# Performance work log

Hardware: AMD Instinct MI355X
Metric: run time of the kernel (lower is better)

## Reference

```python
import jax, jax.numpy as jnp
import numpy as np

WIN = (7, 7)
N_TOK = WIN[0] * WIN[1]          # 49
DIM = 512
HEADS = 16
B_WIN = 2048                     # num_windows * batch
NW = 64                          # windows per image (mask leading dim)


def _relative_position_index():
    # Mirrors the torch __init__ coords computation.
    coords = np.stack(np.meshgrid(np.arange(WIN[0]), np.arange(WIN[1]), indexing='ij'))  # [2,Wh,Ww]
    flat = coords.reshape(2, -1)                                   # [2, N]
    rel = flat[:, :, None] - flat[:, None, :]                      # [2, N, N]
    rel = rel.transpose(1, 2, 0).astype(np.int32)                  # [N, N, 2]
    rel[:, :, 0] += WIN[0] - 1
    rel[:, :, 1] += WIN[1] - 1
    rel[:, :, 0] *= 2 * WIN[1] - 1
    return jnp.asarray(rel.sum(-1), dtype=jnp.int32)               # [N, N]


def setup_inputs() -> dict:
    key = jax.random.key(0)
    ks = jax.random.split(key, 7)
    x = jax.random.normal(ks[0], (B_WIN, N_TOK, DIM), jnp.float32)
    w_qkv = jax.random.normal(ks[1], (3 * DIM, DIM), jnp.float32) * 0.02
    b_qkv = jax.random.normal(ks[2], (3 * DIM,), jnp.float32) * 0.02
    w_proj = jax.random.normal(ks[3], (DIM, DIM), jnp.float32) * 0.02
    b_proj = jax.random.normal(ks[4], (DIM,), jnp.float32) * 0.02
    bias_table = jax.random.normal(ks[5], ((2 * WIN[0] - 1) * (2 * WIN[1] - 1), HEADS), jnp.float32) * 0.02
    rel_index = _relative_position_index()
    # shift-window mask: 0 for allowed, -100 for masked (Swin convention)
    mask = jnp.where(jax.random.bernoulli(ks[6], 0.1, (NW, N_TOK, N_TOK)), -100.0, 0.0).astype(jnp.float32)
    return {"x": x, "w_qkv": w_qkv, "b_qkv": b_qkv, "w_proj": w_proj,
            "b_proj": b_proj, "bias_table": bias_table, "rel_index": rel_index, "mask": mask}


def reference(x, w_qkv, b_qkv, w_proj, b_proj, bias_table, rel_index, mask):
    B_, N, C = x.shape
    H = HEADS
    hd = C // H
    scale = hd ** -0.5
    # qkv projection: [B, N, 3, H, hd] -> q,k,v each [B, H, N, hd]
    qkv = (jnp.einsum('bnc,oc->bno', x, w_qkv) + b_qkv)
    qkv = qkv.reshape(B_, N, 3, H, hd).transpose(2, 0, 3, 1, 4)
    q, k, v = qkv[0], qkv[1], qkv[2]
    attn = jnp.einsum('bhnd,bhmd->bhnm', q * scale, k)             # [B, H, N, N]
    # relative position bias gather: [N*N] -> [N, N, H] -> [H, N, N]
    rpb = bias_table[rel_index.reshape(-1)].reshape(N, N, H).transpose(2, 0, 1)
    attn = attn + rpb[None]
    nW = mask.shape[0]
    attn = attn.reshape(B_ // nW, nW, H, N, N) + mask[None, :, None]
    attn = attn.reshape(B_, H, N, N)
    attn = jax.nn.softmax(attn, axis=-1)
    out = jnp.einsum('bhnm,bhmd->bhnd', attn, v)                   # [B, H, N, hd]
    out = out.transpose(0, 2, 1, 3).reshape(B_, N, C)
    out = jnp.einsum('bnc,oc->bno', out, w_proj) + b_proj
    return out
```

## Files before the change

kernel.cpp:

```cpp
#include <hip/hip_runtime.h>
#include <stdint.h>

typedef unsigned short u16;
typedef unsigned int u32;
typedef unsigned long long u64;
typedef __attribute__((ext_vector_type(4))) u16 u16x4;
typedef __attribute__((ext_vector_type(8))) u16 u16x8;
typedef __attribute__((ext_vector_type(2))) u32 u32x2;
typedef __attribute__((ext_vector_type(8))) short bf16x8;
typedef __attribute__((ext_vector_type(4))) float f32x4;

#define DEVFN __device__ __forceinline__

DEVFN u16 f2bf(float f) {
  union { float f; u32 u; } x; x.f = f;
  u32 u = x.u;
  return (u16)((u + 0x7fffu + ((u >> 16) & 1u)) >> 16);
}
DEVFN float bf2f(u16 v) {
  union { u32 u; float f; } x; x.u = ((u32)v) << 16;
  return x.f;
}

__global__ void cvt_kernel(const float* __restrict__ in, u16* __restrict__ out, int n4) {
  const int stride = gridDim.x * blockDim.x;
  for (int i = blockIdx.x * blockDim.x + threadIdx.x; i < n4; i += stride) {
    float4 v = reinterpret_cast<const float4*>(in)[i];
    u16x4 o;
    o.x = f2bf(v.x); o.y = f2bf(v.y); o.z = f2bf(v.z); o.w = f2bf(v.w);
    reinterpret_cast<u16x4*>(out)[i] = o;
  }
}

__global__ void pbb_kernel(const float* __restrict__ bt, const int* __restrict__ ri,
                           u16* __restrict__ pbb) {
  const int h = blockIdx.x;
  for (int t = threadIdx.x; t < 4096; t += 256) {
    const int i = t >> 6, j = t & 63;
    float v = 0.f;
    if (i < 49 && j < 49) v = bt[ri[i * 49 + j] * 16 + h];
    pbb[h * 4096 + t] = f2bf(v);
  }
}

__global__ void mbits_kernel(const float* __restrict__ mask, u64* __restrict__ mb) {
  const int w = blockIdx.x;
  const int i = threadIdx.x;
  u64 m = ~0ull << 49;
  if (i < 49) {
    for (int j = 0; j < 49; ++j)
      if (mask[w * 2401 + i * 49 + j] < -1.0f) m |= 1ull << j;
  } else {
    m = ~0ull;
  }
  mb[w * 64 + i] = m;
}

#define WAIT_LGKM0 asm volatile("s_waitcnt lgkmcnt(0)" ::: "memory")
#define WAIT_VM8   asm volatile("s_waitcnt vmcnt(8)" ::: "memory")
#define WAIT_VM0   asm volatile("s_waitcnt vmcnt(0)" ::: "memory")
#define SCHEDB     __builtin_amdgcn_sched_barrier(0)
#define BARRIER    __builtin_amdgcn_s_barrier()
#define MFMA(a, b, c) __builtin_amdgcn_mfma_f32_16x16x32_bf16(a, b, c, 0, 0, 0)

template <int MODE, int NTILES, int MCHUNK>
__global__ __launch_bounds__(512) void gemm_kernel(
    const u16* __restrict__ A, const u16* __restrict__ Bt,
    const float* __restrict__ bias, void* __restrict__ Out, int ldo) {
  extern __shared__ u16 smem[];
  const int tid = threadIdx.x;
  const int lane = tid & 63;
  const int wid = tid >> 6;
  const int bid = blockIdx.x;
  const int xcd = bid & 7;
  const int slot = bid >> 3;
  const int m0 = (xcd * MCHUNK + slot / NTILES) * 256;
  const int n0 = (slot % NTILES) * 256;
  const int wr = wid >> 2, wc = wid & 3;
  const int l15 = lane & 15, lg = lane >> 4;
  const int rg0 = tid >> 3;
  const int sl0 = tid & 7;

  f32x4 acc[8][4] = {};

  u16* const sA0 = smem;
  u16* const sB0 = smem + 16384;
  u16* const sA1 = smem + 32768;
  u16* const sB1 = smem + 49152;

#define STAGE(kt_, sa_, sb_)                                                   \
  {                                                                            \
    _Pragma("unroll") for (int i = 0; i < 4; ++i) {                            \
      const int rg = i * 64 + rg0;                                             \
      const int kc = sl0 ^ (rg & 7);                                           \
      const u16* ga = A + (size_t)(m0 + rg) * 512 + (kt_) * 64 + kc * 8;       \
      __builtin_amdgcn_global_load_lds(                                        \
          (const __attribute__((address_space(1))) void*)ga,                   \
          (__attribute__((address_space(3))) void*)((sa_) + i * 4096 + wid * 512), \
          16, 0, 0);                                                           \
    }                                                                          \
    _Pragma("unroll") for (int i = 0; i < 4; ++i) {                            \
      const int rg = i * 64 + rg0;                                             \
      const int kc = sl0 ^ (rg & 7);                                           \
      const u16* gb = Bt + (size_t)(n0 + rg) * 512 + (kt_) * 64 + kc * 8;      \
      __builtin_amdgcn_global_load_lds(                                        \
          (const __attribute__((address_space(1))) void*)gb,                   \
          (__attribute__((address_space(3))) void*)((sb_) + i * 4096 + wid * 512), \
          16, 0, 0);                                                           \
    }                                                                          \
  }

#define RDA(dst, sa_, mi, ks)                                                  \
  {                                                                            \
    const int row_ = wr * 128 + (mi) * 16 + l15;                               \
    dst = *reinterpret_cast<const bf16x8*>(                                    \
        (sa_) + row_ * 64 + ((((ks) * 4 + lg) ^ (row_ & 7)) << 3));            \
  }
#define RDB(dst, sb_, ni, ks)                                                  \
  {                                                                            \
    const int row_ = wc * 64 + (ni) * 16 + l15;                                \
    dst = *reinterpret_cast<const bf16x8*>(                                    \
        (sb_) + row_ * 64 + ((((ks) * 4 + lg) ^ (row_ & 7)) << 3));            \
  }

  STAGE(0, sA0, sB0);
  STAGE(1, sA1, sB1);
  WAIT_VM8; SCHEDB;
  BARRIER; SCHEDB;

#pragma unroll
  for (int kt = 0; kt < 8; ++kt) {
    u16* const sa = (kt & 1) ? sA1 : sA0;
    u16* const sb = (kt & 1) ? sB1 : sB0;
    bf16x8 a0[4][2], a1[4][2], b0[2][2], b1[2][2];

#pragma unroll
    for (int mi = 0; mi < 4; ++mi) { RDA(a0[mi][0], sa, mi, 0); RDA(a0[mi][1], sa, mi, 1); }
#pragma unroll
    for (int ni = 0; ni < 2; ++ni) { RDB(b0[ni][0], sb, ni, 0); RDB(b0[ni][1], sb, ni, 1); }
    WAIT_LGKM0; SCHEDB;
    __builtin_amdgcn_s_setprio(1);
#pragma unroll
    for (int mi = 0; mi < 4; ++mi)
#pragma unroll
      for (int ni = 0; ni < 2; ++ni)
#pragma unroll
        for (int ks = 0; ks < 2; ++ks)
          acc[mi][ni] = MFMA(a0[mi][ks], b0[ni][ks], acc[mi][ni]);
    __builtin_amdgcn_s_setprio(0); SCHEDB;

#pragma unroll
    for (int ni = 0; ni < 2; ++ni) { RDB(b1[ni][0], sb, ni + 2, 0); RDB(b1[ni][1], sb, ni + 2, 1); }
    WAIT_LGKM0; SCHEDB;
    __builtin_amdgcn_s_setprio(1);
#pragma unroll
    for (int mi = 0; mi < 4; ++mi)
#pragma unroll
      for (int ni = 0; ni < 2; ++ni)
#pragma unroll
        for (int ks = 0; ks < 2; ++ks)
          acc[mi][ni + 2] = MFMA(a0[mi][ks], b1[ni][ks], acc[mi][ni + 2]);
    __builtin_amdgcn_s_setprio(0); SCHEDB;

#pragma unroll
    for (int mi = 0; mi < 4; ++mi) { RDA(a1[mi][0], sa, mi + 4, 0); RDA(a1[mi][1], sa, mi + 4, 1); }
    WAIT_LGKM0; SCHEDB;
    __builtin_amdgcn_s_setprio(1);
#pragma unroll
    for (int mi = 0; mi < 4; ++mi)
#pragma unroll
      for (int ni = 0; ni < 2; ++ni)
#pragma unroll
        for (int ks = 0; ks < 2; ++ks)
          acc[mi + 4][ni + 2] = MFMA(a1[mi][ks], b1[ni][ks], acc[mi + 4][ni + 2]);
    __builtin_amdgcn_s_setprio(0); SCHEDB;

    BARRIER; SCHEDB;
    if (kt < 6) STAGE(kt + 2, sa, sb);

    __builtin_amdgcn_s_setprio(1);
#pragma unroll
    for (int mi = 0; mi < 4; ++mi)
#pragma unroll
      for (int ni = 0; ni < 2; ++ni)
#pragma unroll
        for (int ks = 0; ks < 2; ++ks)
          acc[mi + 4][ni] = MFMA(a1[mi][ks], b0[ni][ks], acc[mi + 4][ni]);
    __builtin_amdgcn_s_setprio(0); SCHEDB;

    if (kt < 6) { WAIT_VM8; }
    else if (kt == 6) { WAIT_VM0; }
    SCHEDB;
    if (kt < 7) { BARRIER; SCHEDB; }
  }
#undef STAGE
#undef RDA
#undef RDB

#pragma unroll
  for (int mi = 0; mi < 8; ++mi) {
#pragma unroll
    for (int ni = 0; ni < 4; ++ni) {
      const int col = n0 + wc * 64 + ni * 16 + l15;
      const float bv = bias[col];
      const int rbase = m0 + wr * 128 + mi * 16 + lg * 4;
#pragma unroll
      for (int r = 0; r < 4; ++r) {
        const float v = acc[mi][ni][r] + bv;
        if (MODE == 0) {
          ((u16*)Out)[(size_t)(rbase + r) * ldo + col] = f2bf(v);
        } else {
          ((float*)Out)[(size_t)(rbase + r) * ldo + col] = v;
        }
      }
    }
  }
}

__global__ __launch_bounds__(256) void attn_kernel(
    const u16* __restrict__ qkv, const u16* __restrict__ pbb,
    const u64* __restrict__ mbits, u16* __restrict__ attn_out) {
  const int w = threadIdx.x >> 6;
  const int lane = threadIdx.x & 63;
  const int b = blockIdx.x >> 2;
  const int h = ((blockIdx.x & 3) << 2) | w;
  const int l15 = lane & 15, lg = lane >> 4;
  const int lg4 = lg * 4;

  __shared__ u16 sVT[4][32][72];
  u16 (*vt)[72] = sVT[w];

  for (int i = lane; i < 1152; i += 64) ((u32*)vt)[i] = 0;

  const size_t rowbase = (size_t)b * (49 * 1536) + h * 32;

  for (int c = lane; c < 196; c += 64) {
    const int n = c >> 2, dg = c & 3;
    u16x8 vv = *reinterpret_cast<const u16x8*>(qkv + rowbase + (size_t)n * 1536 + 1024 + dg * 8);
    const int pin = ((n >> 5) << 5) | ((((n >> 2) & 3)) << 3) | (((n >> 4) & 1) << 2) | (n & 3);
#pragma unroll
    for (int j = 0; j < 8; ++j) vt[dg * 8 + j][pin] = vv[j];
  }

  bf16x8 aq[4], bk[4];
#pragma unroll
  for (int t = 0; t < 4; ++t) {
    const int i = t * 16 + l15;
    const int r = i < 49 ? i : 48;
    const size_t ro = rowbase + (size_t)r * 1536 + lg * 8;
    aq[t] = *reinterpret_cast<const bf16x8*>(qkv + ro);
    bk[t] = *reinterpret_cast<const bf16x8*>(qkv + ro + 512);
  }

  const u64* mwb = mbits + ((b & 63) << 6);
  u64 mb[4];
#pragma unroll
  for (int qt = 0; qt < 4; ++qt) mb[qt] = mwb[qt * 16 + l15];

  bf16x8 bv[2][2];
#pragma unroll
  for (int ni = 0; ni < 2; ++ni)
#pragma unroll
    for (int ks = 0; ks < 2; ++ks)
      bv[ni][ks] = *reinterpret_cast<const bf16x8*>(&vt[ni * 16 + l15][ks * 32 + lg * 8]);

  const float scale = 0.17677669529663687f;
  const u16* pbh = pbb + (h << 12);
  const size_t obase = (size_t)b * 49 * 512 + h * 32;

#pragma unroll
  for (int qt = 0; qt < 4; ++qt) {
    f32x4 sT[4] = {};
#pragma unroll
    for (int kt = 0; kt < 4; ++kt)
      sT[kt] = __builtin_amdgcn_mfma_f32_16x16x32_bf16(bk[kt], aq[qt], sT[kt], 0, 0, 0);

    const int i = qt * 16 + l15;
    const u16* pr = pbh + i * 64 + lg4;
    float v[4][4];
    float mx = -3e38f;
#pragma unroll
    for (int kt = 0; kt < 4; ++kt) {
      u16x4 pv = *reinterpret_cast<const u16x4*>(pr + kt * 16);
      const u32 nib = (u32)(mb[qt] >> (kt * 16 + lg4)) & 0xFu;
#pragma unroll
      for (int r = 0; r < 4; ++r) {
        float val = fmaf(sT[kt][r], scale, bf2f(pv[r]));
        if (nib & (1u << r)) val -= 100.f;
        if (kt == 3 && (lg4 + r) >= 1) val = -1e30f;
        v[kt][r] = val;
        mx = fmaxf(mx, val);
      }
    }
    mx = fmaxf(mx, __shfl_xor(mx, 16));
    mx = fmaxf(mx, __shfl_xor(mx, 32));
    float sum = 0.f;
#pragma unroll
    for (int kt = 0; kt < 4; ++kt)
#pragma unroll
      for (int r = 0; r < 4; ++r) {
        const float e = __expf(v[kt][r] - mx);
        v[kt][r] = e;
        sum += e;
      }
    sum += __shfl_xor(sum, 16);
    sum += __shfl_xor(sum, 32);
    const float rinv = 1.0f / sum;

    bf16x8 ap[2];
#pragma unroll
    for (int ks = 0; ks < 2; ++ks) {
      u32 w0 = (u32)f2bf(v[2 * ks][0] * rinv) | ((u32)f2bf(v[2 * ks][1] * rinv) << 16);
      u32 w1 = (u32)f2bf(v[2 * ks][2] * rinv) | ((u32)f2bf(v[2 * ks][3] * rinv) << 16);
      u32 w2 = (u32)f2bf(v[2 * ks + 1][0] * rinv) | ((u32)f2bf(v[2 * ks + 1][1] * rinv) << 16);
      u32 w3 = (u32)f2bf(v[2 * ks + 1][2] * rinv) | ((u32)f2bf(v[2 * ks + 1][3] * rinv) << 16);
      union { u32 u[4]; bf16x8 b; } pk;
      pk.u[0] = w0; pk.u[1] = w1; pk.u[2] = w2; pk.u[3] = w3;
      ap[ks] = pk.b;
    }

    f32x4 o[2] = {};
#pragma unroll
    for (int ks = 0; ks < 2; ++ks)
#pragma unroll
      for (int ni = 0; ni < 2; ++ni)
        o[ni] = __builtin_amdgcn_mfma_f32_16x16x32_bf16(ap[ks], bv[ni][ks], o[ni], 0, 0, 0);

#pragma unroll
    for (int r = 0; r < 4; ++r) {
      const int iq = qt * 16 + lg4 + r;
      if (iq < 49) {
#pragma unroll
        for (int ni = 0; ni < 2; ++ni)
          attn_out[obase + (size_t)iq * 512 + ni * 16 + l15] = f2bf(o[ni][r]);
      }
    }
  }
}

extern "C" void kernel_launch(void* const* d_in, const int* in_sizes, int n_in,
                              void* d_out, int out_size, void* d_ws, size_t ws_size,
                              hipStream_t stream) {
  (void)in_sizes; (void)n_in; (void)out_size; (void)ws_size;
  const float* x          = (const float*)d_in[0];
  const float* w_qkv      = (const float*)d_in[1];
  const float* b_qkv      = (const float*)d_in[2];
  const float* w_proj     = (const float*)d_in[3];
  const float* b_proj     = (const float*)d_in[4];
  const float* bias_table = (const float*)d_in[5];
  const int*   rel_index  = (const int*)d_in[6];
  const float* mask       = (const float*)d_in[7];

  u16* ws     = (u16*)d_ws;
  u16* xbf    = ws;
  u16* qkv    = ws + 51380224;
  u16* wqkvb  = qkv + 154140672;
  u16* wprojb = wqkvb + 786432;
  u16* pbb    = wprojb + 262144;
  u64* mbits  = (u64*)(pbb + 65536);

  (void)hipFuncSetAttribute((const void*)gemm_kernel<0, 6, 49>,
                            hipFuncAttributeMaxDynamicSharedMemorySize, 131072);
  (void)hipFuncSetAttribute((const void*)gemm_kernel<1, 2, 49>,
                            hipFuncAttributeMaxDynamicSharedMemorySize, 131072);

  cvt_kernel<<<2048, 256, 0, stream>>>(x, xbf, 51380224 / 4);
  cvt_kernel<<<192, 256, 0, stream>>>(w_qkv, wqkvb, 786432 / 4);
  cvt_kernel<<<64, 256, 0, stream>>>(w_proj, wprojb, 262144 / 4);
  pbb_kernel<<<16, 256, 0, stream>>>(bias_table, rel_index, pbb);
  mbits_kernel<<<64, 64, 0, stream>>>(mask, mbits);

  gemm_kernel<0, 6, 49><<<2352, 512, 131072, stream>>>(xbf, wqkvb, b_qkv, qkv, 1536);
  attn_kernel<<<8192, 256, 0, stream>>>(qkv, pbb, mbits, xbf);
  gemm_kernel<1, 2, 49><<<784, 512, 131072, stream>>>(xbf, wprojb, b_proj, d_out, 512);
}
```

Measured before the change: 514.2 us.

## Interleave global-to-LDS prefetch in quarter-tile chunks across MFMA phases

Splits each K-tile's global_load_lds staging into four half-panel chunks, issued one per MFMA phase and offset by three phases. The goal is to spread memory traffic evenly across the compute loop rather than issuing all loads at once after a barrier. This adds several extra workgroup barriers per K-step and changes the vmcnt waits. The offset scheduling must avoid overwriting a buffer that is still being read, which is a correctness risk.

```diff
diff --git a/kernel.cpp b/kernel.cpp
--- a/kernel.cpp
+++ b/kernel.cpp
@@ -57,7 +57,8 @@
 }
 
 #define WAIT_LGKM0 asm volatile("s_waitcnt lgkmcnt(0)" ::: "memory")
-#define WAIT_VM8   asm volatile("s_waitcnt vmcnt(8)" ::: "memory")
+#define WAIT_LGKM8 asm volatile("s_waitcnt lgkmcnt(8)" ::: "memory")
+#define WAIT_VM2   asm volatile("s_waitcnt vmcnt(2)" ::: "memory")
 #define WAIT_VM0   asm volatile("s_waitcnt vmcnt(0)" ::: "memory")
 #define SCHEDB     __builtin_amdgcn_sched_barrier(0)
 #define BARRIER    __builtin_amdgcn_s_barrier()
@@ -83,61 +84,62 @@
 
   f32x4 acc[8][4] = {};
 
-  u16* const sA0 = smem;
-  u16* const sB0 = smem + 16384;
-  u16* const sA1 = smem + 32768;
-  u16* const sB1 = smem + 49152;
-
-#define STAGE(kt_, sa_, sb_)                                                   \
+#define STAGE_RAW(kt_, hp_)                                                    \
   {                                                                            \
-    _Pragma("unroll") for (int i = 0; i < 4; ++i) {                            \
-      const int rg = i * 64 + rg0;                                             \
-      const int kc = sl0 ^ (rg & 7);                                           \
-      const u16* ga = A + (size_t)(m0 + rg) * 512 + (kt_) * 64 + kc * 8;       \
+    const u16* srcp_ = ((hp_) < 2)                                             \
+        ? (A + (size_t)(m0 + ((hp_) & 1) * 128) * 512)                         \
+        : (Bt + (size_t)(n0 + ((hp_) & 1) * 128) * 512);                       \
+    u16* dst_ = smem + ((kt_) & 1) * 32768 + (hp_) * 8192;                     \
+    _Pragma("unroll") for (int i_ = 0; i_ < 2; ++i_) {                         \
+      const int rg_ = i_ * 64 + rg0;                                           \
+      const int kc_ = sl0 ^ (rg_ & 7);                                         \
+      const u16* g_ = srcp_ + (size_t)rg_ * 512 + (kt_) * 64 + kc_ * 8;        \
       __builtin_amdgcn_global_load_lds(                                        \
-          (const __attribute__((address_space(1))) void*)ga,                   \
-          (__attribute__((address_space(3))) void*)((sa_) + i * 4096 + wid * 512), \
+          (const __attribute__((address_space(1))) void*)g_,                   \
+          (__attribute__((address_space(3))) void*)(dst_ + i_ * 4096 + wid * 512), \
           16, 0, 0);                                                           \
     }                                                                          \
-    _Pragma("unroll") for (int i = 0; i < 4; ++i) {                            \
-      const int rg = i * 64 + rg0;                                             \
-      const int kc = sl0 ^ (rg & 7);                                           \
-      const u16* gb = Bt + (size_t)(n0 + rg) * 512 + (kt_) * 64 + kc * 8;      \
-      __builtin_amdgcn_global_load_lds(                                        \
-          (const __attribute__((address_space(1))) void*)gb,                   \
-          (__attribute__((address_space(3))) void*)((sb_) + i * 4096 + wid * 512), \
-          16, 0, 0);                                                           \
-    }                                                                          \
-  }
-
-#define RDA(dst, sa_, mi, ks)                                                  \
+  }
+
+#define STG(g_)                                                                \
+  if ((g_) >= 3 && (g_) < 27) {                                                \
+    const int s_ = (g_) - 3;                                                   \
+    STAGE_RAW(2 + s_ / 4, s_ & 3);                                             \
+  }
+
+#define RDA(dst, mi_, ks_)                                                     \
   {                                                                            \
-    const int row_ = wr * 128 + (mi) * 16 + l15;                               \
+    const int row_ = wr * 128 + (mi_) * 16 + l15;                              \
     dst = *reinterpret_cast<const bf16x8*>(                                    \
-        (sa_) + row_ * 64 + ((((ks) * 4 + lg) ^ (row_ & 7)) << 3));            \
-  }
-#define RDB(dst, sb_, ni, ks)                                                  \
+        smem + cb + row_ * 64 + ((((ks_) * 4 + lg) ^ (row_ & 7)) << 3));       \
+  }
+#define RDB(dst, ni_, ks_)                                                     \
   {                                                                            \
-    const int row_ = wc * 64 + (ni) * 16 + l15;                                \
+    const int row_ = wc * 64 + (ni_) * 16 + l15;                               \
     dst = *reinterpret_cast<const bf16x8*>(                                    \
-        (sb_) + row_ * 64 + ((((ks) * 4 + lg) ^ (row_ & 7)) << 3));            \
-  }
-
-  STAGE(0, sA0, sB0);
-  STAGE(1, sA1, sB1);
-  WAIT_VM8; SCHEDB;
+        smem + cb + 16384 + row_ * 64 + ((((ks_) * 4 + lg) ^ (row_ & 7)) << 3)); \
+  }
+
+#pragma unroll
+  for (int hp = 0; hp < 4; ++hp) STAGE_RAW(0, hp);
+#pragma unroll
+  for (int hp = 0; hp < 4; ++hp) STAGE_RAW(1, hp);
+  WAIT_VM0; SCHEDB;
   BARRIER; SCHEDB;
 
 #pragma unroll
   for (int kt = 0; kt < 8; ++kt) {
-    u16* const sa = (kt & 1) ? sA1 : sA0;
-    u16* const sb = (kt & 1) ? sB1 : sB0;
+    const int cb = (kt & 1) * 32768;
+    const int g0 = kt * 4;
     bf16x8 a0[4][2], a1[4][2], b0[2][2], b1[2][2];
 
 #pragma unroll
-    for (int mi = 0; mi < 4; ++mi) { RDA(a0[mi][0], sa, mi, 0); RDA(a0[mi][1], sa, mi, 1); }
-#pragma unroll
-    for (int ni = 0; ni < 2; ++ni) { RDB(b0[ni][0], sb, ni, 0); RDB(b0[ni][1], sb, ni, 1); }
+    for (int mi = 0; mi < 4; ++mi) { RDA(a0[mi][0], mi, 0); RDA(a0[mi][1], mi, 1); }
+#pragma unroll
+    for (int ni = 0; ni < 2; ++ni) { RDB(b0[ni][0], ni, 0); RDB(b0[ni][1], ni, 1); }
+    STG(g0 + 0);
+    WAIT_LGKM8; SCHEDB;
+    BARRIER;
     WAIT_LGKM0; SCHEDB;
     __builtin_amdgcn_s_setprio(1);
 #pragma unroll
@@ -148,9 +150,12 @@
         for (int ks = 0; ks < 2; ++ks)
           acc[mi][ni] = MFMA(a0[mi][ks], b0[ni][ks], acc[mi][ni]);
     __builtin_amdgcn_s_setprio(0); SCHEDB;
-
-#pragma unroll
-    for (int ni = 0; ni < 2; ++ni) { RDB(b1[ni][0], sb, ni + 2, 0); RDB(b1[ni][1], sb, ni + 2, 1); }
+    BARRIER; SCHEDB;
+
+#pragma unroll
+    for (int ni = 0; ni < 2; ++ni) { RDB(b1[ni][0], ni + 2, 0); RDB(b1[ni][1], ni + 2, 1); }
+    STG(g0 + 1);
+    BARRIER;
     WAIT_LGKM0; SCHEDB;
     __builtin_amdgcn_s_setprio(1);
 #pragma unroll
@@ -161,9 +166,12 @@
         for (int ks = 0; ks < 2; ++ks)
           acc[mi][ni + 2] = MFMA(a0[mi][ks], b1[ni][ks], acc[mi][ni + 2]);
     __builtin_amdgcn_s_setprio(0); SCHEDB;
-
-#pragma unroll
-    for (int mi = 0; mi < 4; ++mi) { RDA(a1[mi][0], sa, mi + 4, 0); RDA(a1[mi][1], sa, mi + 4, 1); }
+    BARRIER; SCHEDB;
+
+#pragma unroll
+    for (int mi = 0; mi < 4; ++mi) { RDA(a1[mi][0], mi + 4, 0); RDA(a1[mi][1], mi + 4, 1); }
+    STG(g0 + 2);
+    BARRIER;
     WAIT_LGKM0; SCHEDB;
     __builtin_amdgcn_s_setprio(1);
 #pragma unroll
@@ -174,10 +182,10 @@
         for (int ks = 0; ks < 2; ++ks)
           acc[mi + 4][ni + 2] = MFMA(a1[mi][ks], b1[ni][ks], acc[mi + 4][ni + 2]);
     __builtin_amdgcn_s_setprio(0); SCHEDB;
-
-    BARRIER; SCHEDB;
-    if (kt < 6) STAGE(kt + 2, sa, sb);
-
+    BARRIER; SCHEDB;
+
+    STG(g0 + 3);
+    BARRIER; SCHEDB;
     __builtin_amdgcn_s_setprio(1);
 #pragma unroll
     for (int mi = 0; mi < 4; ++mi)
@@ -187,13 +195,13 @@
         for (int ks = 0; ks < 2; ++ks)
           acc[mi + 4][ni] = MFMA(a1[mi][ks], b0[ni][ks], acc[mi + 4][ni]);
     __builtin_amdgcn_s_setprio(0); SCHEDB;
-
-    if (kt < 6) { WAIT_VM8; }
-    else if (kt == 6) { WAIT_VM0; }
+    if (g0 + 3 == 27) { WAIT_VM0; }
+    else if (g0 + 3 < 27) { WAIT_VM2; }
     SCHEDB;
-    if (kt < 7) { BARRIER; SCHEDB; }
-  }
-#undef STAGE
+    BARRIER; SCHEDB;
+  }
+#undef STAGE_RAW
+#undef STG
 #undef RDA
 #undef RDB
 
```

Result: no change. 505.4 us (-1.7%).

## Halve GEMM K-tile to 32 and shrink LDS to allow two blocks per CU

Applied to the files above, without the earlier changes.

The GEMM K tile drops from 64 to 32, giving 16 pipeline steps instead of 8. LDS swizzling changes to a 4-slot XOR pattern to match, and the interleaved sub-phase MFMA schedule becomes a single load-all-fragments-then-compute step. Dynamic LDS per block is halved, which could let two 512-thread blocks share a CU and hide latency. The trade-off is twice as many barriers and waits per K loop and less latency hiding within each block.

```diff
diff --git a/kernel.cpp b/kernel.cpp
--- a/kernel.cpp
+++ b/kernel.cpp
@@ -57,7 +57,7 @@
 }
 
 #define WAIT_LGKM0 asm volatile("s_waitcnt lgkmcnt(0)" ::: "memory")
-#define WAIT_VM8   asm volatile("s_waitcnt vmcnt(8)" ::: "memory")
+#define WAIT_VM4   asm volatile("s_waitcnt vmcnt(4)" ::: "memory")
 #define WAIT_VM0   asm volatile("s_waitcnt vmcnt(0)" ::: "memory")
 #define SCHEDB     __builtin_amdgcn_sched_barrier(0)
 #define BARRIER    __builtin_amdgcn_s_barrier()
@@ -78,124 +78,76 @@
   const int n0 = (slot % NTILES) * 256;
   const int wr = wid >> 2, wc = wid & 3;
   const int l15 = lane & 15, lg = lane >> 4;
-  const int rg0 = tid >> 3;
-  const int sl0 = tid & 7;
+  const int rg0 = tid >> 2;
+  const int sl0 = tid & 3;
 
   f32x4 acc[8][4] = {};
 
-  u16* const sA0 = smem;
-  u16* const sB0 = smem + 16384;
-  u16* const sA1 = smem + 32768;
-  u16* const sB1 = smem + 49152;
-
-#define STAGE(kt_, sa_, sb_)                                                   \
+#define STAGE(kt_)                                                             \
   {                                                                            \
-    _Pragma("unroll") for (int i = 0; i < 4; ++i) {                            \
-      const int rg = i * 64 + rg0;                                             \
-      const int kc = sl0 ^ (rg & 7);                                           \
-      const u16* ga = A + (size_t)(m0 + rg) * 512 + (kt_) * 64 + kc * 8;       \
+    const int bb_ = ((kt_) & 1) * 16384;                                       \
+    _Pragma("unroll") for (int i_ = 0; i_ < 2; ++i_) {                         \
+      const int rg_ = i_ * 128 + rg0;                                          \
+      const int kc_ = sl0 ^ (rg_ & 3) ^ ((rg_ >> 2) & 3);                      \
+      const u16* g_ = A + (size_t)(m0 + rg_) * 512 + (kt_) * 32 + kc_ * 8;     \
       __builtin_amdgcn_global_load_lds(                                        \
-          (const __attribute__((address_space(1))) void*)ga,                   \
-          (__attribute__((address_space(3))) void*)((sa_) + i * 4096 + wid * 512), \
+          (const __attribute__((address_space(1))) void*)g_,                   \
+          (__attribute__((address_space(3))) void*)(smem + bb_ + i_ * 4096 +   \
+                                                    wid * 512),                \
           16, 0, 0);                                                           \
     }                                                                          \
-    _Pragma("unroll") for (int i = 0; i < 4; ++i) {                            \
-      const int rg = i * 64 + rg0;                                             \
-      const int kc = sl0 ^ (rg & 7);                                           \
-      const u16* gb = Bt + (size_t)(n0 + rg) * 512 + (kt_) * 64 + kc * 8;      \
+    _Pragma("unroll") for (int i_ = 0; i_ < 2; ++i_) {                         \
+      const int rg_ = i_ * 128 + rg0;                                          \
+      const int kc_ = sl0 ^ (rg_ & 3) ^ ((rg_ >> 2) & 3);                      \
+      const u16* g_ = Bt + (size_t)(n0 + rg_) * 512 + (kt_) * 32 + kc_ * 8;    \
       __builtin_amdgcn_global_load_lds(                                        \
-          (const __attribute__((address_space(1))) void*)gb,                   \
-          (__attribute__((address_space(3))) void*)((sb_) + i * 4096 + wid * 512), \
+          (const __attribute__((address_space(1))) void*)g_,                   \
+          (__attribute__((address_space(3))) void*)(smem + bb_ + 8192 +        \
+                                                    i_ * 4096 + wid * 512),    \
           16, 0, 0);                                                           \
     }                                                                          \
   }
 
-#define RDA(dst, sa_, mi, ks)                                                  \
-  {                                                                            \
-    const int row_ = wr * 128 + (mi) * 16 + l15;                               \
-    dst = *reinterpret_cast<const bf16x8*>(                                    \
-        (sa_) + row_ * 64 + ((((ks) * 4 + lg) ^ (row_ & 7)) << 3));            \
-  }
-#define RDB(dst, sb_, ni, ks)                                                  \
-  {                                                                            \
-    const int row_ = wc * 64 + (ni) * 16 + l15;                                \
-    dst = *reinterpret_cast<const bf16x8*>(                                    \
-        (sb_) + row_ * 64 + ((((ks) * 4 + lg) ^ (row_ & 7)) << 3));            \
-  }
-
-  STAGE(0, sA0, sB0);
-  STAGE(1, sA1, sB1);
-  WAIT_VM8; SCHEDB;
+  STAGE(0);
+  STAGE(1);
+  WAIT_VM4; SCHEDB;
   BARRIER; SCHEDB;
 
 #pragma unroll
-  for (int kt = 0; kt < 8; ++kt) {
-    u16* const sa = (kt & 1) ? sA1 : sA0;
-    u16* const sb = (kt & 1) ? sB1 : sB0;
-    bf16x8 a0[4][2], a1[4][2], b0[2][2], b1[2][2];
-
-#pragma unroll
-    for (int mi = 0; mi < 4; ++mi) { RDA(a0[mi][0], sa, mi, 0); RDA(a0[mi][1], sa, mi, 1); }
-#pragma unroll
-    for (int ni = 0; ni < 2; ++ni) { RDB(b0[ni][0], sb, ni, 0); RDB(b0[ni][1], sb, ni, 1); }
-    WAIT_LGKM0; SCHEDB;
+  for (int t = 0; t < 16; ++t) {
+    const int cb = (t & 1) * 16384;
+    bf16x8 af[8], bfr[4];
+#pragma unroll
+    for (int mi = 0; mi < 8; ++mi) {
+      const int row = wr * 128 + mi * 16 + l15;
+      const int sl = lg ^ (row & 3) ^ ((row >> 2) & 3);
+      af[mi] = *reinterpret_cast<const bf16x8*>(smem + cb + row * 32 + sl * 8);
+    }
+#pragma unroll
+    for (int ni = 0; ni < 4; ++ni) {
+      const int row = wc * 64 + ni * 16 + l15;
+      const int sl = lg ^ (row & 3) ^ ((row >> 2) & 3);
+      bfr[ni] = *reinterpret_cast<const bf16x8*>(smem + cb + 8192 + row * 32 + sl * 8);
+    }
+    WAIT_LGKM0;
+    SCHEDB;
+    BARRIER;
+    SCHEDB;
+    if (t < 14) STAGE(t + 2);
     __builtin_amdgcn_s_setprio(1);
 #pragma unroll
-    for (int mi = 0; mi < 4; ++mi)
-#pragma unroll
-      for (int ni = 0; ni < 2; ++ni)
-#pragma unroll
-        for (int ks = 0; ks < 2; ++ks)
-          acc[mi][ni] = MFMA(a0[mi][ks], b0[ni][ks], acc[mi][ni]);
-    __builtin_amdgcn_s_setprio(0); SCHEDB;
-
-#pragma unroll
-    for (int ni = 0; ni < 2; ++ni) { RDB(b1[ni][0], sb, ni + 2, 0); RDB(b1[ni][1], sb, ni + 2, 1); }
-    WAIT_LGKM0; SCHEDB;
-    __builtin_amdgcn_s_setprio(1);
-#pragma unroll
-    for (int mi = 0; mi < 4; ++mi)
-#pragma unroll
-      for (int ni = 0; ni < 2; ++ni)
-#pragma unroll
-        for (int ks = 0; ks < 2; ++ks)
-          acc[mi][ni + 2] = MFMA(a0[mi][ks], b1[ni][ks], acc[mi][ni + 2]);
-    __builtin_amdgcn_s_setprio(0); SCHEDB;
-
-#pragma unroll
-    for (int mi = 0; mi < 4; ++mi) { RDA(a1[mi][0], sa, mi + 4, 0); RDA(a1[mi][1], sa, mi + 4, 1); }
-    WAIT_LGKM0; SCHEDB;
-    __builtin_amdgcn_s_setprio(1);
-#pragma unroll
-    for (int mi = 0; mi < 4; ++mi)
-#pragma unroll
-      for (int ni = 0; ni < 2; ++ni)
-#pragma unroll
-        for (int ks = 0; ks < 2; ++ks)
-          acc[mi + 4][ni + 2] = MFMA(a1[mi][ks], b1[ni][ks], acc[mi + 4][ni + 2]);
-    __builtin_amdgcn_s_setprio(0); SCHEDB;
-
-    BARRIER; SCHEDB;
-    if (kt < 6) STAGE(kt + 2, sa, sb);
-
-    __builtin_amdgcn_s_setprio(1);
-#pragma unroll
-    for (int mi = 0; mi < 4; ++mi)
-#pragma unroll
-      for (int ni = 0; ni < 2; ++ni)
-#pragma unroll
-        for (int ks = 0; ks < 2; ++ks)
-          acc[mi + 4][ni] = MFMA(a1[mi][ks], b0[ni][ks], acc[mi + 4][ni]);
-    __builtin_amdgcn_s_setprio(0); SCHEDB;
-
-    if (kt < 6) { WAIT_VM8; }
-    else if (kt == 6) { WAIT_VM0; }
+    for (int mi = 0; mi < 8; ++mi)
+#pragma unroll
+      for (int ni = 0; ni < 4; ++ni)
+        acc[mi][ni] = MFMA(af[mi], bfr[ni], acc[mi][ni]);
+    __builtin_amdgcn_s_setprio(0);
     SCHEDB;
-    if (kt < 7) { BARRIER; SCHEDB; }
+    if (t < 14) { WAIT_VM4; }
+    else if (t == 14) { WAIT_VM0; }
+    SCHEDB;
+    if (t < 15) { BARRIER; SCHEDB; }
   }
 #undef STAGE
-#undef RDA
-#undef RDB
 
 #pragma unroll
   for (int mi = 0; mi < 8; ++mi) {
@@ -360,9 +312,9 @@
   u64* mbits  = (u64*)(pbb + 65536);
 
   (void)hipFuncSetAttribute((const void*)gemm_kernel<0, 6, 49>,
-                            hipFuncAttributeMaxDynamicSharedMemorySize, 131072);
+                            hipFuncAttributeMaxDynamicSharedMemorySize, 65536);
   (void)hipFuncSetAttribute((const void*)gemm_kernel<1, 2, 49>,
-                            hipFuncAttributeMaxDynamicSharedMemorySize, 131072);
+                            hipFuncAttributeMaxDynamicSharedMemorySize, 65536);
 
   cvt_kernel<<<2048, 256, 0, stream>>>(x, xbf, 51380224 / 4);
   cvt_kernel<<<192, 256, 0, stream>>>(w_qkv, wqkvb, 786432 / 4);
@@ -370,7 +322,7 @@
   pbb_kernel<<<16, 256, 0, stream>>>(bias_table, rel_index, pbb);
   mbits_kernel<<<64, 64, 0, stream>>>(mask, mbits);
 
-  gemm_kernel<0, 6, 49><<<2352, 512, 131072, stream>>>(xbf, wqkvb, b_qkv, qkv, 1536);
+  gemm_kernel<0, 6, 49><<<2352, 512, 65536, stream>>>(xbf, wqkvb, b_qkv, qkv, 1536);
   attn_kernel<<<8192, 256, 0, stream>>>(qkv, pbb, mbits, xbf);
-  gemm_kernel<1, 2, 49><<<784, 512, 131072, stream>>>(xbf, wprojb, b_proj, d_out, 512);
-}
+  gemm_kernel<1, 2, 49><<<784, 512, 65536, stream>>>(xbf, wprojb, b_proj, d_out, 512);
+}
```

Result: slower. 542.8 us (+5.6%).
